# Performance work log

Hardware: AMD Instinct MI355X
Metric: run time of the kernel (lower is better)

Reference implementation:

```python
import jax, jax.numpy as jnp
import numpy as np
from jax import lax

EPS = 1e-5

def setup_inputs() -> dict:
    key = jax.random.key(0)
    ks = jax.random.split(key, 8)
    B, D, H, W = 2, 96, 96, 96
    K, N, R = 4, 16, 6
    return {
        "x": jax.random.normal(ks[0], (B, D, H, W), jnp.float32),
        "x_proj_weight": jax.random.normal(ks[1], (K, R + 2 * N, D), jnp.float32) * 0.05,
        "dt_projs_weight": jax.random.normal(ks[2], (K, D, R), jnp.float32) * 0.05,
        "dt_projs_bias": jax.random.normal(ks[3], (K, D), jnp.float32) * 0.05,
        "A_logs": jax.random.uniform(ks[4], (K * D, N), jnp.float32, 0.0, 1.0),
        "Ds": jax.random.normal(ks[5], (K * D,), jnp.float32) * 0.1,
        "norm_weight": jnp.ones((D,), jnp.float32),
        "norm_bias": jnp.zeros((D,), jnp.float32),
    }

def _cross_scan(x):
    # x: [B,C,H,W] -> xs: [B,4,C,L]; dirs: row-major, col-major, and their flips
    B, C, H, W = x.shape
    x_hw = x.reshape(B, C, H * W)
    x_wh = jnp.swapaxes(x, 2, 3).reshape(B, C, H * W)
    return jnp.stack([x_hw, x_wh, x_hw[..., ::-1], x_wh[..., ::-1]], axis=1)

def _cross_merge(ys, H, W):
    # ys: [B,4,C,L] -> y: [B,C,L]
    B, K, C, L = ys.shape
    ys = ys[:, 0:2] + ys[:, 2:4][..., ::-1]
    y_wh = jnp.swapaxes(ys[:, 1].reshape(B, C, W, H), 2, 3).reshape(B, C, L)
    return ys[:, 0] + y_wh

def _forward(x, x_proj_weight, dt_projs_weight, dt_projs_bias, A_logs, Ds,
             norm_weight, norm_bias):
    B, D, H, W = x.shape
    L = H * W
    K, _, R = dt_projs_weight.shape
    N = A_logs.shape[1]

    xs = _cross_scan(x)                                        # [B,K,D,L]
    x_dbl = jnp.einsum('bkdl,kcd->bkcl', xs, x_proj_weight)    # [B,K,R+2N,L]
    dts, Bs, Cs = x_dbl[:, :, :R], x_dbl[:, :, R:R + N], x_dbl[:, :, R + N:]
    dts = jnp.einsum('bkrl,kdr->bkdl', dts, dt_projs_weight)   # [B,K,D,L]

    A = -jnp.exp(A_logs).reshape(K, D, N)                      # [K,D,N]
    delta = jax.nn.softplus(dts + dt_projs_bias[None, :, :, None])  # [B,K,D,L]

    # time-major for scan
    u_t = jnp.moveaxis(xs, 3, 0)       # [L,B,K,D]
    d_t = jnp.moveaxis(delta, 3, 0)    # [L,B,K,D]
    B_t = jnp.moveaxis(Bs, 3, 0)       # [L,B,K,N]
    C_t = jnp.moveaxis(Cs, 3, 0)       # [L,B,K,N]

    def step(h, inp):
        u, dlt, b, c = inp
        h = jnp.exp(dlt[..., None] * A) * h + (dlt * u)[..., None] * b[:, :, None, :]
        y = jnp.einsum('bkdn,bkn->bkd', h, c)
        return h, y

    h0 = jnp.zeros((B, K, D, N), xs.dtype)
    _, ys = lax.scan(step, h0, (u_t, d_t, B_t, C_t))           # ys: [L,B,K,D]
    ys = jnp.moveaxis(ys, 0, 3)                                # [B,K,D,L]
    ys = ys + Ds.reshape(1, K, D, 1) * xs                      # skip term

    y = _cross_merge(ys, H, W)                                 # [B,D,L]
    y = jnp.swapaxes(y, 1, 2)                                  # [B,L,D]
    # out_norm: LayerNorm over channel dim
    mu = y.mean(-1, keepdims=True)
    var = y.var(-1, keepdims=True)
    y = (y - mu) / jnp.sqrt(var + EPS) * norm_weight + norm_bias
    return y.reshape(B, H, W, D)

def reference(x, x_proj_weight, dt_projs_weight, dt_projs_bias, A_logs, Ds,
              norm_weight, norm_bias):
    return _forward(x, x_proj_weight, dt_projs_weight, dt_projs_bias,
                    A_logs, Ds, norm_weight, norm_bias)
```

## Files before the change

kernel.cpp:

```cpp
#include <hip/hip_runtime.h>
#include <hip/hip_bf16.h>
#include <hip/hip_fp16.h>


constexpr int Bn = 2, Kn = 4, Dn = 96, Hn = 96, Wn = 96, Ln = Hn * Wn;
constexpr int Nn = 16, Rn = 6;
constexpr int CCn = 144, CLn = 64;

#define DI __device__ __forceinline__

typedef _Float16 half2v __attribute__((ext_vector_type(2)));

DI float bf2f(unsigned short u) { return __uint_as_float(((unsigned)u) << 16); }
DI bool probe_bf16(const void* nw) { return ((const unsigned*)nw)[0] == 0x3F803F80u; }
DI float ld_in(const void* p, long i, bool bf) {
  return bf ? bf2f(((const unsigned short*)p)[i]) : ((const float*)p)[i];
}
DI float fexp2(float x) {
#if __has_builtin(__builtin_amdgcn_exp2f)
  return __builtin_amdgcn_exp2f(x);
#else
  return exp2f(x);
#endif
}
DI float softplus_fast(float v) {
  return (v > 15.f) ? v : __logf(1.f + __expf(v));
}
DI float dot2acc(unsigned a, unsigned b, float c) {
#if __has_builtin(__builtin_amdgcn_fdot2)
  half2v av, bv;
  __builtin_memcpy(&av, &a, 4);
  __builtin_memcpy(&bv, &b, 4);
  return __builtin_amdgcn_fdot2(av, bv, c, false);
#else
  __half2 ah = *(__half2*)&a, bh = *(__half2*)&b;
  float2 af = __half22float2(ah), bf2_ = __half22float2(bh);
  return fmaf(af.y, bf2_.y, fmaf(af.x, bf2_.x, c));
#endif
}
DI float quad_reduce_add(float v) {
  int a = __builtin_amdgcn_mov_dpp(__float_as_int(v), 0xB1, 0xF, 0xF, true);
  v += __int_as_float(a);
  int b = __builtin_amdgcn_mov_dpp(__float_as_int(v), 0x4E, 0xF, 0xF, true);
  v += __int_as_float(b);
  return v;
}
constexpr float LOG2E = 1.44269504088896340736f;

__global__ __launch_bounds__(256) void k_prep(
    const void* __restrict__ x, const void* __restrict__ xpw,
    const void* __restrict__ dtw, const void* __restrict__ dtb,
    const void* __restrict__ Al, const void* __restrict__ Ds,
    const void* __restrict__ nw, const void* __restrict__ nb,
    float* __restrict__ xl, float* __restrict__ xlT,
    float* __restrict__ wp_f, float* __restrict__ wdt_f,
    float* __restrict__ bias_f, float* __restrict__ Al_f,
    float* __restrict__ dsum, float* __restrict__ nw_f, float* __restrict__ nb_f) {
  __shared__ float tile[96 * 97];
  bool bf = probe_bf16(nw);
  int h = blockIdx.x, b = blockIdx.y;
  int tid = threadIdx.x;
  int fi = (blockIdx.y * gridDim.x + blockIdx.x) * 256 + tid;
  int fgs = gridDim.x * gridDim.y * 256;
  for (int i = fi; i < Kn * 38 * Dn; i += fgs) wp_f[i] = ld_in(xpw, i, bf);
  for (int i = fi; i < Kn * Dn * Rn; i += fgs) wdt_f[i] = ld_in(dtw, i, bf);
  for (int i = fi; i < Kn * Dn; i += fgs) bias_f[i] = ld_in(dtb, i, bf);
  for (int i = fi; i < Kn * Dn * Nn; i += fgs)
    Al_f[i] = -__expf(ld_in(Al, i, bf)) * LOG2E;
  for (int i = fi; i < Dn; i += fgs) {
    dsum[i] = ld_in(Ds, i, bf) + ld_in(Ds, 96 + i, bf) +
              ld_in(Ds, 192 + i, bf) + ld_in(Ds, 288 + i, bf);
    nw_f[i] = ld_in(nw, i, bf);
    nb_f[i] = ld_in(nb, i, bf);
  }
  long srcbase = (long)b * Dn * Ln + (long)h * 96;
  for (int i = tid; i < 96 * 96; i += 256) {
    int d = i / 96, w = i - d * 96;
    tile[d * 97 + w] = ld_in(x, srcbase + (long)d * Ln + w, bf);
  }
  __syncthreads();
  float* xlb = xl + (size_t)b * Ln * 96;
  float* xTb = xlT + (size_t)b * Ln * 96;
  for (int i = tid; i < 96 * 96; i += 256) {
    int w = i / 96, d = i - w * 96;
    float v = tile[d * 97 + w];
    xlb[(size_t)(h * 96 + w) * 96 + d] = v;
    xTb[(size_t)(w * 96 + h) * 96 + d] = v;
  }
}

__global__ __launch_bounds__(256) void k_proj(
    const float* __restrict__ xl, const float* __restrict__ xlT,
    const float* __restrict__ wp_f, const float* __restrict__ wdt_f,
    const float* __restrict__ bias_f,
    __half2* __restrict__ ddu, __half* __restrict__ BCh) {
  constexpr int TL = 64;
  __shared__ __half xt[TL * 102];
  __shared__ __half wp[40 * 100];
  __shared__ __half xd2[TL * 40];
  __shared__ unsigned wdt_u[96 * 4];
  __shared__ float bias[96];
  int tile = blockIdx.x, k = blockIdx.y, b = blockIdx.z;
  int l0 = tile * TL;
  int tid = threadIdx.x;
  bool rev = (k & 2) != 0;

  for (int i = tid; i < 40 * 100; i += 256) {
    int c = i / 100, dd = i - c * 100;
    wp[i] = __float2half((c < 38 && dd < 96) ? wp_f[k * 38 * 96 + c * 96 + dd]
                                             : 0.f);
  }
  for (int i = tid; i < 96 * 3; i += 256) {
    int d = i / 3, rr = i - d * 3;
    __half2 hv = __floats2half2_rn(wdt_f[k * 576 + d * 6 + rr * 2],
                                   wdt_f[k * 576 + d * 6 + rr * 2 + 1]);
    wdt_u[d * 4 + rr] = *(unsigned*)&hv;
  }
  if (tid < 96) bias[tid] = bias_f[k * 96 + tid];
  {
    const float* xsrc = ((k & 1) ? xlT : xl) + (size_t)b * Ln * 96;
    for (int i = tid; i < TL * 24; i += 256) {
      int r = i / 24, q = i - r * 24;
      int g = rev ? (Ln - 1 - l0 - r) : (l0 + r);
      float4 v = *(const float4*)(xsrc + (size_t)g * 96 + q * 4);
      *(__half2*)(&xt[r * 102 + q * 4]) = __floats2half2_rn(v.x, v.y);
      *(__half2*)(&xt[r * 102 + q * 4 + 2]) = __floats2half2_rn(v.z, v.w);
    }
  }
  __syncthreads();

  {
    int jg = tid & 31, cg = tid >> 5;
    int j0 = jg * 2, c0 = cg * 5;
    float acc[5][2];
#pragma unroll
    for (int i = 0; i < 5; ++i) { acc[i][0] = 0.f; acc[i][1] = 0.f; }
    for (int dd = 0; dd < 96; dd += 4) {
      uint2 xa = *(const uint2*)&xt[(j0 + 0) * 102 + dd];
      uint2 xb = *(const uint2*)&xt[(j0 + 1) * 102 + dd];
#pragma unroll
      for (int i = 0; i < 5; ++i) {
        uint2 wv = *(const uint2*)&wp[(c0 + i) * 100 + dd];
        acc[i][0] = dot2acc(xa.x, wv.x, acc[i][0]);
        acc[i][0] = dot2acc(xa.y, wv.y, acc[i][0]);
        acc[i][1] = dot2acc(xb.x, wv.x, acc[i][1]);
        acc[i][1] = dot2acc(xb.y, wv.y, acc[i][1]);
      }
    }
#pragma unroll
    for (int i = 0; i < 5; ++i) {
      xd2[j0 * 40 + c0 + i] = __float2half(acc[i][0]);
      xd2[(j0 + 1) * 40 + c0 + i] = __float2half(acc[i][1]);
    }
  }
  __syncthreads();

  size_t bk = (size_t)b * 4 + k;
  {
    __half2* o = (__half2*)(BCh + (bk * (size_t)Ln + l0) * 32);
    for (int i = tid; i < TL * 16; i += 256) {
      int j = i >> 4, cp = i & 15;
      int c = cp * 2;
      int ng = c >> 3, idx = c & 7;
      int ch = (idx < 4) ? (6 + ng * 4 + idx) : (22 + ng * 4 + (idx - 4));
      o[i] = *(const __half2*)&xd2[j * 40 + ch];
    }
  }
  {
    int lp = tid >> 2, q = tid & 3, d0 = q * 24;
    uint2 xr01 = *(const uint2*)&xd2[lp * 40];
    unsigned xr2 = *(const unsigned*)&xd2[lp * 40 + 4];
    __half2* orow = ddu + (bk * (size_t)Ln + l0 + lp) * 96 + d0;
#pragma unroll
    for (int ii = 0; ii < 6; ++ii) {
      union { uint4 u4; __half2 h2[4]; } pk;
      __half2 u01 = *(const __half2*)&xt[lp * 102 + d0 + ii * 4];
      __half2 u23 = *(const __half2*)&xt[lp * 102 + d0 + ii * 4 + 2];
      float2 uf01 = __half22float2(u01), uf23 = __half22float2(u23);
      float uv[4] = {uf01.x, uf01.y, uf23.x, uf23.y};
#pragma unroll
      for (int p = 0; p < 4; ++p) {
        int d = d0 + ii * 4 + p;
        uint2 wv = *(const uint2*)&wdt_u[d * 4];
        unsigned wv2 = wdt_u[d * 4 + 2];
        float v = dot2acc(xr01.x, wv.x,
                  dot2acc(xr01.y, wv.y,
                  dot2acc(xr2, wv2, bias[d])));
        float sp = softplus_fast(v);
        pk.h2[p] = __floats2half2_rn(sp, sp * uv[p]);
      }
      *(uint4*)(orow + ii * 4) = pk.u4;
    }
  }
}

__global__ __launch_bounds__(192) void k_scan1(
    const __half2* __restrict__ ddu, const __half* __restrict__ BCh,
    const float* __restrict__ Al_f, float* __restrict__ PSg) {
  __shared__ __half2 dd_s[CLn * 96];
  __shared__ __half b_s[CLn * 16];
  int chunk = blockIdx.x, k = blockIdx.y, b = blockIdx.z;
  int tid = threadIdx.x;
  int dp = tid >> 2, ng = tid & 3;
  int d0 = dp * 2, n0 = ng * 4;
  int bk = b * 4 + k;
  int t0 = chunk * CLn;
  float ac[2][4];
#pragma unroll
  for (int dd = 0; dd < 2; ++dd)
#pragma unroll
    for (int j = 0; j < 4; ++j)
      ac[dd][j] = Al_f[(k * 96 + d0 + dd) * 16 + n0 + j];
  {
    const uint4* dsrc = (const uint4*)(ddu + ((size_t)bk * Ln + t0) * 96);
    uint4* ddst = (uint4*)dd_s;
    for (int i = tid; i < CLn * 96 / 4; i += 192) ddst[i] = dsrc[i];
    const uint2* bsrc = (const uint2*)(BCh + ((size_t)bk * Ln + t0) * 32);
    uint2* bdst = (uint2*)b_s;
    for (int i = tid; i < CLn * 4; i += 192) {
      int t = i >> 2, g = i & 3;
      bdst[t * 4 + g] = bsrc[t * 8 + g * 2];
    }
  }
  __syncthreads();

  float P[2][4] = {{1.f, 1.f, 1.f, 1.f}, {1.f, 1.f, 1.f, 1.f}};
  float S[2][4] = {{0.f, 0.f, 0.f, 0.f}, {0.f, 0.f, 0.f, 0.f}};
#pragma unroll 2
  for (int t = 0; t < CLn; ++t) {
    union { uint2 u; __half2 h2[2]; } dv;
    dv.u = *(const uint2*)&dd_s[t * 96 + d0];
    union { uint2 u; __half2 h2[2]; } bv;
    bv.u = *(const uint2*)&b_s[t * 16 + n0];
    float2 f0 = __half22float2(dv.h2[0]);
    float2 f1 = __half22float2(dv.h2[1]);
    float2 B01 = __half22float2(bv.h2[0]);
    float2 B23 = __half22float2(bv.h2[1]);
    float Ba[4] = {B01.x, B01.y, B23.x, B23.y};
#pragma unroll
    for (int j = 0; j < 4; ++j) {
      float a0 = fexp2(f0.x * ac[0][j]);
      P[0][j] *= a0;
      S[0][j] = fmaf(a0, S[0][j], f0.y * Ba[j]);
      float a1 = fexp2(f1.x * ac[1][j]);
      P[1][j] *= a1;
      S[1][j] = fmaf(a1, S[1][j], f1.y * Ba[j]);
    }
  }
  size_t ob0 = ((size_t)(bk * 96 + d0) * CCn + chunk) * 32 + n0;
  size_t ob1 = ((size_t)(bk * 96 + d0 + 1) * CCn + chunk) * 32 + n0;
  *(float4*)(PSg + ob0) = make_float4(P[0][0], P[0][1], P[0][2], P[0][3]);
  *(float4*)(PSg + ob0 + 16) = make_float4(S[0][0], S[0][1], S[0][2], S[0][3]);
  *(float4*)(PSg + ob1) = make_float4(P[1][0], P[1][1], P[1][2], P[1][3]);
  *(float4*)(PSg + ob1 + 16) = make_float4(S[1][0], S[1][1], S[1][2], S[1][3]);
}

__global__ __launch_bounds__(256) void k_midscan(float* __restrict__ PSg) {
  __shared__ float Pl[256], Sl[256];
  int bkd = blockIdx.x;
  int tid = threadIdx.x;
  int g = tid >> 4, n = tid & 15;
  constexpr int CPG = CCn / 16;
  size_t base = ((size_t)bkd * CCn + (size_t)g * CPG) * 32 + n;
  float Pr[CPG], Sr[CPG];
#pragma unroll
  for (int i = 0; i < CPG; ++i) {
    Pr[i] = PSg[base + (size_t)i * 32];
    Sr[i] = PSg[base + (size_t)i * 32 + 16];
  }
  float Pa = 1.f, Sa = 0.f;
#pragma unroll
  for (int i = 0; i < CPG; ++i) { Sa = fmaf(Pr[i], Sa, Sr[i]); Pa *= Pr[i]; }
  Pl[tid] = Pa;
  Sl[tid] = Sa;
  __syncthreads();
#pragma unroll
  for (int s = 1; s < 16; s <<= 1) {
    float Pp = 1.f, Sp = 0.f;
    if (g >= s) { Pp = Pl[(g - s) * 16 + n]; Sp = Sl[(g - s) * 16 + n]; }
    __syncthreads();
    if (g >= s) {
      Sl[tid] = fmaf(Pl[tid], Sp, Sl[tid]);
      Pl[tid] *= Pp;
    }
    __syncthreads();
  }
  float h = (g == 0) ? 0.f : Sl[(g - 1) * 16 + n];
#pragma unroll
  for (int i = 0; i < CPG; ++i) {
    PSg[base + (size_t)i * 32] = h;
    h = fmaf(Pr[i], h, Sr[i]);
  }
}

__global__ __launch_bounds__(192) void k_scan2(
    const __half2* __restrict__ ddu, const __half* __restrict__ BCh,
    const float* __restrict__ Al_f, const float* __restrict__ PSg,
    __half* __restrict__ ysH) {
  __shared__ __half2 dd_s[CLn * 96];
  __shared__ __half bc_s[CLn * 32];
  int chunk = blockIdx.x, k = blockIdx.y, b = blockIdx.z;
  int tid = threadIdx.x;
  int dp = tid >> 2, ng = tid & 3;
  int d0 = dp * 2, n0 = ng * 4;
  int bk = b * 4 + k;
  int t0 = chunk * CLn;
  float ac[2][4];
#pragma unroll
  for (int dd = 0; dd < 2; ++dd)
#pragma unroll
    for (int j = 0; j < 4; ++j)
      ac[dd][j] = Al_f[(k * 96 + d0 + dd) * 16 + n0 + j];
  {
    const uint4* dsrc = (const uint4*)(ddu + ((size_t)bk * Ln + t0) * 96);
    uint4* ddst = (uint4*)dd_s;
    for (int i = tid; i < CLn * 96 / 4; i += 192) ddst[i] = dsrc[i];
    const uint4* bsrc = (const uint4*)(BCh + ((size_t)bk * Ln + t0) * 32);
    uint4* bdst = (uint4*)bc_s;
    for (int i = tid; i < CLn * 32 * 2 / 16; i += 192) bdst[i] = bsrc[i];
  }
  float4 ha = *(const float4*)(PSg + ((size_t)(bk * 96 + d0) * CCn + chunk) * 32 + n0);
  float4 hb = *(const float4*)(PSg + ((size_t)(bk * 96 + d0 + 1) * CCn + chunk) * 32 + n0);
  float h[2][4] = {{ha.x, ha.y, ha.z, ha.w}, {hb.x, hb.y, hb.z, hb.w}};
  __syncthreads();

#pragma unroll 2
  for (int t = 0; t < CLn; ++t) {
    union { uint2 u; __half2 h2[2]; } dv;
    dv.u = *(const uint2*)&dd_s[t * 96 + d0];
    union { uint4 u; __half2 h2[4]; } bc;
    bc.u = *(const uint4*)&bc_s[t * 32 + ng * 8];
    float2 f0 = __half22float2(dv.h2[0]);
    float2 f1 = __half22float2(dv.h2[1]);
    float2 b01 = __half22float2(bc.h2[0]);
    float2 b23 = __half22float2(bc.h2[1]);
    float2 c01 = __half22float2(bc.h2[2]);
    float2 c23 = __half22float2(bc.h2[3]);
    float Ba[4] = {b01.x, b01.y, b23.x, b23.y};
    float Ca[4] = {c01.x, c01.y, c23.x, c23.y};
    float py0 = 0.f, py1 = 0.f;
#pragma unroll
    for (int j = 0; j < 4; ++j) {
      float a0 = fexp2(f0.x * ac[0][j]);
      h[0][j] = fmaf(a0, h[0][j], f0.y * Ba[j]);
      py0 = fmaf(h[0][j], Ca[j], py0);
      float a1 = fexp2(f1.x * ac[1][j]);
      h[1][j] = fmaf(a1, h[1][j], f1.y * Ba[j]);
      py1 = fmaf(h[1][j], Ca[j], py1);
    }
    py0 = quad_reduce_add(py0);
    py1 = quad_reduce_add(py1);
    if (ng == 0)
      *(__half2*)&ysH[((size_t)bk * Ln + t0 + t) * 96 + d0] =
          __halves2half2(__float2half(py0), __float2half(py1));
  }
}

__global__ __launch_bounds__(256) void k_merge_ln(
    const __half* __restrict__ ysH, const float* __restrict__ xl,
    const float* __restrict__ dsum, const void* __restrict__ nwraw,
    const float* __restrict__ nw_f, const float* __restrict__ nb_f,
    void* __restrict__ outv) {
  __shared__ float yt[64 * 98];
  __shared__ float nwf[96], nbf[96], dsm[96], mu_s[64], rs_s[64];
  bool bf = probe_bf16(nwraw);
  int tile = blockIdx.x, b = blockIdx.y;
  int h0 = (tile / 12) * 8, w0 = (tile % 12) * 8;
  int tid = threadIdx.x;
  if (tid < 96) {
    nwf[tid] = nw_f[tid];
    nbf[tid] = nb_f[tid];
    dsm[tid] = dsum[tid];
  }
  const __half* y0 = ysH + (size_t)(b * 4 + 0) * Ln * 96;
  const __half* y1 = ysH + (size_t)(b * 4 + 1) * Ln * 96;
  const __half* y2 = ysH + (size_t)(b * 4 + 2) * Ln * 96;
  const __half* y3 = ysH + (size_t)(b * 4 + 3) * Ln * 96;
  const float* xb = xl + (size_t)b * Ln * 96;
  __syncthreads();
  for (int i = tid; i < 64 * 48; i += 256) {
    int rr = i / 48, dp = i - rr * 48, d = dp * 2;
    int hh = h0 + (rr >> 3), ww = w0 + (rr & 7);
    int l = hh * 96 + ww, t1 = ww * 96 + hh;
    float2 v0 = __half22float2(*(const __half2*)&y0[(size_t)l * 96 + d]);
    float2 v1 = __half22float2(*(const __half2*)&y1[(size_t)t1 * 96 + d]);
    float2 v2 = __half22float2(*(const __half2*)&y2[(size_t)(Ln - 1 - l) * 96 + d]);
    float2 v3 = __half22float2(*(const __half2*)&y3[(size_t)(Ln - 1 - t1) * 96 + d]);
    float2 xv = *(const float2*)&xb[(size_t)l * 96 + d];
    float2 r;
    r.x = v0.x + v1.x + v2.x + v3.x + dsm[d] * xv.x;
    r.y = v0.y + v1.y + v2.y + v3.y + dsm[d + 1] * xv.y;
    *(float2*)&yt[rr * 98 + d] = r;
  }
  __syncthreads();
  {
    int rr = tid >> 2, qq = tid & 3;
    float s = 0.f, ss = 0.f;
#pragma unroll 4
    for (int d2 = 0; d2 < 24; ++d2) {
      float v = yt[rr * 98 + qq * 24 + d2];
      s += v;
      ss += v * v;
    }
    s = quad_reduce_add(s);
    ss = quad_reduce_add(ss);
    if (qq == 0) {
      float mu = s * (1.f / 96.f);
      float var = fmaxf(ss * (1.f / 96.f) - mu * mu, 0.f);
      mu_s[rr] = mu;
      rs_s[rr] = rsqrtf(var + 1e-5f);
    }
  }
  __syncthreads();
  for (int i = tid; i < 64 * 48; i += 256) {
    int rr = i / 48, dp = i - rr * 48, d = dp * 2;
    int hh = h0 + (rr >> 3), ww = w0 + (rr & 7);
    size_t idx = ((size_t)b * Ln + hh * 96 + ww) * 96 + d;
    float2 yv = *(const float2*)&yt[rr * 98 + d];
    float mu = mu_s[rr], rs = rs_s[rr];
    float o0 = (yv.x - mu) * rs * nwf[d] + nbf[d];
    float o1 = (yv.y - mu) * rs * nwf[d + 1] + nbf[d + 1];
    if (bf) {
      union { unsigned u; unsigned short us[2]; } pk;
      __hip_bfloat16 b0 = __float2bfloat16(o0), b1 = __float2bfloat16(o1);
      pk.us[0] = *(unsigned short*)&b0;
      pk.us[1] = *(unsigned short*)&b1;
      *(unsigned*)&((__hip_bfloat16*)outv)[idx] = pk.u;
    } else {
      *(float2*)&((float*)outv)[idx] = make_float2(o0, o1);
    }
  }
}

extern "C" void kernel_launch(void* const* d_in, const int* in_sizes, int n_in,
                              void* d_out, int out_size, void* d_ws, size_t ws_size,
                              hipStream_t stream) {
  const void* x   = d_in[0];
  const void* xpw = d_in[1];
  const void* dtw = d_in[2];
  const void* dtb = d_in[3];
  const void* Al  = d_in[4];
  const void* Ds  = d_in[5];
  const void* nw  = d_in[6];
  const void* nb  = d_in[7];

  char* ws = (char*)d_ws;
  size_t off = 0;
  auto alloc = [&](size_t bytes) {
    char* p = ws + off;
    off += (bytes + 511) & ~(size_t)511;
    return p;
  };
  float* xl    = (float*)alloc((size_t)Bn * Ln * Dn * 4);
  float* xlT   = (float*)alloc((size_t)Bn * Ln * Dn * 4);
  float* wp_f  = (float*)alloc((size_t)Kn * 38 * Dn * 4);
  float* wdt_f = (float*)alloc((size_t)Kn * Dn * Rn * 4);
  float* bias_f= (float*)alloc((size_t)Kn * Dn * 4);
  float* Al_f  = (float*)alloc((size_t)Kn * Dn * Nn * 4);
  float* dsum  = (float*)alloc((size_t)Dn * 4);
  float* nw_f  = (float*)alloc((size_t)Dn * 4);
  float* nb_f  = (float*)alloc((size_t)Dn * 4);
  __half2* ddu = (__half2*)alloc((size_t)Bn * Kn * Ln * Dn * 4);
  __half* BCh  = (__half*)alloc((size_t)Bn * Kn * Ln * 32 * 2);
  float* PS    = (float*)alloc((size_t)Bn * Kn * Dn * CCn * 32 * 4);
  __half* ysH  = (__half*)alloc((size_t)Bn * Kn * Ln * Dn * 2);
  (void)ws_size; (void)in_sizes; (void)n_in; (void)out_size;

  k_prep<<<dim3(Hn, Bn), dim3(256), 0, stream>>>(
      x, xpw, dtw, dtb, Al, Ds, nw, nb, xl, xlT, wp_f, wdt_f, bias_f, Al_f,
      dsum, nw_f, nb_f);
  k_proj<<<dim3(Ln / 64, Kn, Bn), dim3(256), 0, stream>>>(xl, xlT, wp_f, wdt_f,
                                                          bias_f, ddu, BCh);
  k_scan1<<<dim3(CCn, Kn, Bn), dim3(192), 0, stream>>>(ddu, BCh, Al_f, PS);
  k_midscan<<<dim3(Bn * Kn * Dn), dim3(256), 0, stream>>>(PS);
  k_scan2<<<dim3(CCn, Kn, Bn), dim3(192), 0, stream>>>(ddu, BCh, Al_f, PS, ysH);
  k_merge_ln<<<dim3(144, Bn), dim3(256), 0, stream>>>(ysH, xl, dsum, nw, nw_f,
                                                      nb_f, d_out);
}
```

Measured before the change: 196.5 us.

## Fuse chunk-local scan pass into projection kernel using shared-memory results

The per-chunk prefix scan (P,S products) now runs at the end of k_proj, on the delta/delta*u values kept in shared memory and the B values already in xd2. The separate k_scan1 launch and its global reload of ddu and BCh go away. This adds 24 KB of shared memory per block, which may cut occupancy of the projection kernel. The serial scan tail also uses only 192 of 256 threads.

```diff
diff --git a/kernel.cpp b/kernel.cpp
--- a/kernel.cpp
+++ b/kernel.cpp
@@ -92,14 +92,16 @@
 __global__ __launch_bounds__(256) void k_proj(
     const float* __restrict__ xl, const float* __restrict__ xlT,
     const float* __restrict__ wp_f, const float* __restrict__ wdt_f,
-    const float* __restrict__ bias_f,
-    __half2* __restrict__ ddu, __half* __restrict__ BCh) {
+    const float* __restrict__ bias_f, const float* __restrict__ Al_f,
+    __half2* __restrict__ ddu, __half* __restrict__ BCh,
+    float* __restrict__ PSg) {
   constexpr int TL = 64;
   __shared__ __half xt[TL * 102];
   __shared__ __half wp[40 * 100];
   __shared__ __half xd2[TL * 40];
   __shared__ unsigned wdt_u[96 * 4];
   __shared__ float bias[96];
+  __shared__ __half2 dd_l[TL * 96];
   int tile = blockIdx.x, k = blockIdx.y, b = blockIdx.z;
   int l0 = tile * TL;
   int tid = threadIdx.x;
@@ -190,69 +192,39 @@
         pk.h2[p] = __floats2half2_rn(sp, sp * uv[p]);
       }
       *(uint4*)(orow + ii * 4) = pk.u4;
-    }
-  }
-}
-
-__global__ __launch_bounds__(192) void k_scan1(
-    const __half2* __restrict__ ddu, const __half* __restrict__ BCh,
-    const float* __restrict__ Al_f, float* __restrict__ PSg) {
-  __shared__ __half2 dd_s[CLn * 96];
-  __shared__ __half b_s[CLn * 16];
-  int chunk = blockIdx.x, k = blockIdx.y, b = blockIdx.z;
-  int tid = threadIdx.x;
-  int dp = tid >> 2, ng = tid & 3;
-  int d0 = dp * 2, n0 = ng * 4;
-  int bk = b * 4 + k;
-  int t0 = chunk * CLn;
-  float ac[2][4];
-#pragma unroll
-  for (int dd = 0; dd < 2; ++dd)
-#pragma unroll
-    for (int j = 0; j < 4; ++j)
-      ac[dd][j] = Al_f[(k * 96 + d0 + dd) * 16 + n0 + j];
-  {
-    const uint4* dsrc = (const uint4*)(ddu + ((size_t)bk * Ln + t0) * 96);
-    uint4* ddst = (uint4*)dd_s;
-    for (int i = tid; i < CLn * 96 / 4; i += 192) ddst[i] = dsrc[i];
-    const uint2* bsrc = (const uint2*)(BCh + ((size_t)bk * Ln + t0) * 32);
-    uint2* bdst = (uint2*)b_s;
-    for (int i = tid; i < CLn * 4; i += 192) {
-      int t = i >> 2, g = i & 3;
-      bdst[t * 4 + g] = bsrc[t * 8 + g * 2];
-    }
-  }
-  __syncthreads();
-
-  float P[2][4] = {{1.f, 1.f, 1.f, 1.f}, {1.f, 1.f, 1.f, 1.f}};
-  float S[2][4] = {{0.f, 0.f, 0.f, 0.f}, {0.f, 0.f, 0.f, 0.f}};
+      *(uint4*)&dd_l[lp * 96 + d0 + ii * 4] = pk.u4;
+    }
+  }
+  __syncthreads();
+
+  if (tid < 192) {
+    int d = tid >> 1, hg = tid & 1;
+    float ac2[8];
+    *(float4*)&ac2[0] = *(const float4*)&Al_f[(k * 96 + d) * 16 + hg * 8];
+    *(float4*)&ac2[4] = *(const float4*)&Al_f[(k * 96 + d) * 16 + hg * 8 + 4];
+    float P[8] = {1.f, 1.f, 1.f, 1.f, 1.f, 1.f, 1.f, 1.f};
+    float S[8] = {0.f, 0.f, 0.f, 0.f, 0.f, 0.f, 0.f, 0.f};
 #pragma unroll 2
-  for (int t = 0; t < CLn; ++t) {
-    union { uint2 u; __half2 h2[2]; } dv;
-    dv.u = *(const uint2*)&dd_s[t * 96 + d0];
-    union { uint2 u; __half2 h2[2]; } bv;
-    bv.u = *(const uint2*)&b_s[t * 16 + n0];
-    float2 f0 = __half22float2(dv.h2[0]);
-    float2 f1 = __half22float2(dv.h2[1]);
-    float2 B01 = __half22float2(bv.h2[0]);
-    float2 B23 = __half22float2(bv.h2[1]);
-    float Ba[4] = {B01.x, B01.y, B23.x, B23.y};
-#pragma unroll
-    for (int j = 0; j < 4; ++j) {
-      float a0 = fexp2(f0.x * ac[0][j]);
-      P[0][j] *= a0;
-      S[0][j] = fmaf(a0, S[0][j], f0.y * Ba[j]);
-      float a1 = fexp2(f1.x * ac[1][j]);
-      P[1][j] *= a1;
-      S[1][j] = fmaf(a1, S[1][j], f1.y * Ba[j]);
-    }
-  }
-  size_t ob0 = ((size_t)(bk * 96 + d0) * CCn + chunk) * 32 + n0;
-  size_t ob1 = ((size_t)(bk * 96 + d0 + 1) * CCn + chunk) * 32 + n0;
-  *(float4*)(PSg + ob0) = make_float4(P[0][0], P[0][1], P[0][2], P[0][3]);
-  *(float4*)(PSg + ob0 + 16) = make_float4(S[0][0], S[0][1], S[0][2], S[0][3]);
-  *(float4*)(PSg + ob1) = make_float4(P[1][0], P[1][1], P[1][2], P[1][3]);
-  *(float4*)(PSg + ob1 + 16) = make_float4(S[1][0], S[1][1], S[1][2], S[1][3]);
+    for (int t = 0; t < TL; ++t) {
+      float2 f = __half22float2(dd_l[t * 96 + d]);
+#pragma unroll
+      for (int w = 0; w < 4; ++w) {
+        __half2 bh = *(const __half2*)&xd2[t * 40 + 6 + hg * 8 + w * 2];
+        float2 Bv = __half22float2(bh);
+        float a0 = fexp2(f.x * ac2[w * 2]);
+        P[w * 2] *= a0;
+        S[w * 2] = fmaf(a0, S[w * 2], f.y * Bv.x);
+        float a1 = fexp2(f.x * ac2[w * 2 + 1]);
+        P[w * 2 + 1] *= a1;
+        S[w * 2 + 1] = fmaf(a1, S[w * 2 + 1], f.y * Bv.y);
+      }
+    }
+    size_t ob = ((size_t)(bk * 96 + d) * CCn + tile) * 32 + hg * 8;
+    *(float4*)&PSg[ob] = make_float4(P[0], P[1], P[2], P[3]);
+    *(float4*)&PSg[ob + 4] = make_float4(P[4], P[5], P[6], P[7]);
+    *(float4*)&PSg[ob + 16] = make_float4(S[0], S[1], S[2], S[3]);
+    *(float4*)&PSg[ob + 20] = make_float4(S[4], S[5], S[6], S[7]);
+  }
 }
 
 __global__ __launch_bounds__(256) void k_midscan(float* __restrict__ PSg) {
@@ -469,9 +441,8 @@
   k_prep<<<dim3(Hn, Bn), dim3(256), 0, stream>>>(
       x, xpw, dtw, dtb, Al, Ds, nw, nb, xl, xlT, wp_f, wdt_f, bias_f, Al_f,
       dsum, nw_f, nb_f);
-  k_proj<<<dim3(Ln / 64, Kn, Bn), dim3(256), 0, stream>>>(xl, xlT, wp_f, wdt_f,
-                                                          bias_f, ddu, BCh);
-  k_scan1<<<dim3(CCn, Kn, Bn), dim3(192), 0, stream>>>(ddu, BCh, Al_f, PS);
+  k_proj<<<dim3(Ln / 64, Kn, Bn), dim3(256), 0, stream>>>(
+      xl, xlT, wp_f, wdt_f, bias_f, Al_f, ddu, BCh, PS);
   k_midscan<<<dim3(Bn * Kn * Dn), dim3(256), 0, stream>>>(PS);
   k_scan2<<<dim3(CCn, Kn, Bn), dim3(192), 0, stream>>>(ddu, BCh, Al_f, PS, ysH);
   k_merge_ln<<<dim3(144, Bn), dim3(256), 0, stream>>>(ysH, xl, dsum, nw, nw_f,
```

After: 194.5 us. No clear change (-1.0%).
